# Performance work log

Hardware: AMD Instinct MI355X
Metric: run time of the kernel (lower is better)

Reference implementation:

```python
import jax, jax.numpy as jnp
import numpy as np

NUM_HEADS = 32
HEAD_DIM = 128
ROPE_THETA = 10000.0


def setup_inputs() -> dict:
    key = jax.random.key(0)
    k1, k2, k3 = jax.random.split(key, 3)
    B, S, H = 2, 2048, 4096
    scale = 0.02
    return {
        "x": jax.random.normal(k1, (B, S, H), dtype=jnp.float32),
        "Wqkv": jax.random.normal(k2, (H, 3 * H), dtype=jnp.float32) * scale,
        "Wo": jax.random.normal(k3, (H, H), dtype=jnp.float32) * scale,
    }


def _rope_cos_sin(seq_len, head_dim, dtype):
    # inv_freq over even dims, llama convention
    inv_freq = 1.0 / (ROPE_THETA ** (jnp.arange(0, head_dim, 2, dtype=jnp.float32) / head_dim))
    t = jnp.arange(seq_len, dtype=jnp.float32)
    freqs = jnp.outer(t, inv_freq)            # [S, hd/2]
    emb = jnp.concatenate([freqs, freqs], -1)  # [S, hd]
    return jnp.cos(emb).astype(dtype), jnp.sin(emb).astype(dtype)


def _rotate_half(v):
    v1, v2 = jnp.split(v, 2, axis=-1)
    return jnp.concatenate([-v2, v1], axis=-1)


def _apply_rope(q, k, cos, sin):
    # q,k: [B,S,nh,hd]; cos,sin: [S,hd] -> broadcast over B and heads
    cos = cos[None, :, None, :]
    sin = sin[None, :, None, :]
    q = q * cos + _rotate_half(q) * sin
    k = k * cos + _rotate_half(k) * sin
    return q, k


def reference(x, Wqkv, Wo):
    B, S, H = x.shape
    nh, hd = NUM_HEADS, HEAD_DIM
    scaling = 1.0 / jnp.sqrt(jnp.asarray(hd, dtype=x.dtype))

    qkv = jnp.einsum("bsh,hk->bsk", x, Wqkv)           # fused QKV proj
    q, k, v = jnp.split(qkv, 3, axis=-1)
    q = q.reshape(B, S, nh, hd)
    k = k.reshape(B, S, nh, hd)
    v = v.reshape(B, S, nh, hd)

    cos, sin = _rope_cos_sin(S, hd, x.dtype)
    q, k = _apply_rope(q, k, cos, sin)

    # causal scaled dot-product attention
    scores = jnp.einsum("bqnd,bknd->bnqk", q, k) * scaling  # [B,nh,S,S]
    causal = jnp.tril(jnp.ones((S, S), dtype=bool))
    scores = jnp.where(causal[None, None], scores, jnp.finfo(scores.dtype).min)
    probs = jax.nn.softmax(scores, axis=-1)
    ctx = jnp.einsum("bnqk,bknd->bqnd", probs, v).reshape(B, S, nh * hd)

    return jnp.einsum("bsh,ho->bso", ctx, Wo)
```

## Files before the change

kernel.cpp:

```cpp
#include <hip/hip_runtime.h>

typedef __bf16 v8bf __attribute__((ext_vector_type(8)));
typedef float  v4f  __attribute__((ext_vector_type(4)));

__device__ __forceinline__ float bf2f(unsigned short h) {
    union { unsigned int u; float f; } x; x.u = ((unsigned int)h) << 16; return x.f;
}
__device__ __forceinline__ unsigned short f2bf(float f) {
    union { float f; unsigned int u; } x; x.f = f;
    unsigned int u = x.u;
    u += 0x7fffu + ((u >> 16) & 1u);
    return (unsigned short)(u >> 16);
}
__device__ __forceinline__ void gll16(const void* g, void* l) {
    __builtin_amdgcn_global_load_lds((__attribute__((address_space(1))) void*)g,
                                     (__attribute__((address_space(3))) void*)l,
                                     16, 0, 0);
}

__global__ __launch_bounds__(256) void cvt_f32_bf16(
    const float* __restrict__ in, unsigned short* __restrict__ out)
{
    size_t i = ((size_t)blockIdx.x * 256 + threadIdx.x) * 4;
    float4 v = *(const float4*)&in[i];
    ushort4 o;
    o.x = f2bf(v.x); o.y = f2bf(v.y); o.z = f2bf(v.z); o.w = f2bf(v.w);
    *(ushort4*)&out[i] = o;
}

__global__ __launch_bounds__(256) void transpose_f32_bf16(
    const float* __restrict__ in, unsigned short* __restrict__ out, int ldIn, int M)
{
    __shared__ unsigned short t[64][68];
    const int c0 = blockIdx.x * 64, r0 = blockIdx.y * 64;
    const int lr = threadIdx.x >> 4;
    const int lc = (threadIdx.x & 15) * 4;
#pragma unroll
    for (int i = 0; i < 4; ++i) {
        int row = lr + i * 16;
        float4 v = *(const float4*)&in[(size_t)(r0 + row) * ldIn + c0 + lc];
        ushort4 o;
        o.x = f2bf(v.x); o.y = f2bf(v.y); o.z = f2bf(v.z); o.w = f2bf(v.w);
        *(ushort4*)&t[row][lc] = o;
    }
    __syncthreads();
#pragma unroll
    for (int i = 0; i < 4; ++i) {
        int orow = lr + i * 16;
        ushort4 v;
        v.x = t[lc + 0][orow]; v.y = t[lc + 1][orow];
        v.z = t[lc + 2][orow]; v.w = t[lc + 3][orow];
        *(ushort4*)&out[(size_t)(c0 + orow) * M + r0 + lc] = v;
    }
}

template <int MODE>
__global__ __launch_bounds__(512, 2) void gemm256(
    const unsigned short* __restrict__ A, const unsigned short* __restrict__ Bt,
    float* __restrict__ Cf, unsigned short* __restrict__ Ov, float postScale)
{
    constexpr int NT = 128;
    __shared__ unsigned short lA[4][8192];
    __shared__ unsigned short lB[4][8192];
    const int tid = threadIdx.x;
    const int wave = tid >> 6, lane = tid & 63;
    const int quad = lane >> 4, l16 = lane & 15;
    const int wr = wave >> 2, wc = wave & 3;

    const int bid = blockIdx.x;
    const int swz = (bid & 7) * 32 + (bid >> 3);
    const int m0 = (swz >> 4) * 256, n0 = (swz & 15) * 256;

    v4f acc[8][4] = {};

    const int sr0 = tid >> 2, sc0 = tid & 3;
    const int sr1 = 128 + sr0;
    const unsigned short* pA0 = A  + (size_t)(m0 + sr0) * 4096 + ((sc0 ^ ((sr0 >> 1) & 3)) << 3);
    const unsigned short* pA1 = A  + (size_t)(m0 + sr1) * 4096 + ((sc0 ^ ((sr1 >> 1) & 3)) << 3);
    const unsigned short* pB0 = Bt + (size_t)(n0 + sr0) * 4096 + ((sc0 ^ ((sr0 >> 1) & 3)) << 3);
    const unsigned short* pB1 = Bt + (size_t)(n0 + sr1) * 4096 + ((sc0 ^ ((sr1 >> 1) & 3)) << 3);

    {
        gll16(pA0, &lA[0][tid * 8]);  gll16(pA1, &lA[0][4096 + tid * 8]);
        gll16(pB0, &lB[0][tid * 8]);  gll16(pB1, &lB[0][4096 + tid * 8]);
        gll16(pA0 + 32, &lA[1][tid * 8]);  gll16(pA1 + 32, &lA[1][4096 + tid * 8]);
        gll16(pB0 + 32, &lB[1][tid * 8]);  gll16(pB1 + 32, &lB[1][4096 + tid * 8]);
        gll16(pA0 + 64, &lA[2][tid * 8]);  gll16(pA1 + 64, &lA[2][4096 + tid * 8]);
        gll16(pB0 + 64, &lB[2][tid * 8]);  gll16(pB1 + 64, &lB[2][4096 + tid * 8]);
    }
    asm volatile("s_waitcnt vmcnt(8)" ::: "memory");
    __builtin_amdgcn_s_barrier();

    const int swzk = (l16 >> 1) & 3;
    const int aoff = (wr * 128 + l16) * 32 + ((quad ^ swzk) << 3);
    const int boff = (wc * 16  + l16) * 32 + ((quad ^ swzk) << 3);

#pragma unroll 4
    for (int t = 0; t < NT; ++t) {
        const int cur = t & 3;
        const int nb = (t + 3) & 3;
        const size_t ko = (size_t)(t + 3) << 5;
        const bool pf = (t + 3 < NT);
        const unsigned short* lAc = &lA[cur][0];
        const unsigned short* lBc = &lB[cur][0];
        v8bf b[4], a0, a1;

        b[0] = *(const v8bf*)&lBc[boff];
        b[1] = *(const v8bf*)&lBc[boff + 2048];
        b[2] = *(const v8bf*)&lBc[boff + 4096];
        b[3] = *(const v8bf*)&lBc[boff + 6144];
        a0 = *(const v8bf*)&lAc[aoff];
        a1 = *(const v8bf*)&lAc[aoff + 512];
        if (pf) gll16(pA0 + ko, &lA[nb][tid * 8]);
        __builtin_amdgcn_s_barrier();
        __builtin_amdgcn_s_setprio(1);
#pragma unroll
        for (int ni = 0; ni < 4; ++ni) {
            acc[0][ni] = __builtin_amdgcn_mfma_f32_16x16x32_bf16(a0, b[ni], acc[0][ni], 0, 0, 0);
            acc[1][ni] = __builtin_amdgcn_mfma_f32_16x16x32_bf16(a1, b[ni], acc[1][ni], 0, 0, 0);
        }
        __builtin_amdgcn_s_setprio(0);

        a0 = *(const v8bf*)&lAc[aoff + 1024];
        a1 = *(const v8bf*)&lAc[aoff + 1536];
        if (pf) gll16(pA1 + ko, &lA[nb][4096 + tid * 8]);
        __builtin_amdgcn_s_barrier();
        __builtin_amdgcn_s_setprio(1);
#pragma unroll
        for (int ni = 0; ni < 4; ++ni) {
            acc[2][ni] = __builtin_amdgcn_mfma_f32_16x16x32_bf16(a0, b[ni], acc[2][ni], 0, 0, 0);
            acc[3][ni] = __builtin_amdgcn_mfma_f32_16x16x32_bf16(a1, b[ni], acc[3][ni], 0, 0, 0);
        }
        __builtin_amdgcn_s_setprio(0);

        a0 = *(const v8bf*)&lAc[aoff + 2048];
        a1 = *(const v8bf*)&lAc[aoff + 2560];
        if (pf) gll16(pB0 + ko, &lB[nb][tid * 8]);
        __builtin_amdgcn_s_barrier();
        __builtin_amdgcn_s_setprio(1);
#pragma unroll
        for (int ni = 0; ni < 4; ++ni) {
            acc[4][ni] = __builtin_amdgcn_mfma_f32_16x16x32_bf16(a0, b[ni], acc[4][ni], 0, 0, 0);
            acc[5][ni] = __builtin_amdgcn_mfma_f32_16x16x32_bf16(a1, b[ni], acc[5][ni], 0, 0, 0);
        }
        __builtin_amdgcn_s_setprio(0);

        a0 = *(const v8bf*)&lAc[aoff + 3072];
        a1 = *(const v8bf*)&lAc[aoff + 3584];
        if (pf) gll16(pB1 + ko, &lB[nb][4096 + tid * 8]);
        if (t < NT - 3)       asm volatile("s_waitcnt vmcnt(8)" ::: "memory");
        else if (t == NT - 3) asm volatile("s_waitcnt vmcnt(4)" ::: "memory");
        else if (t == NT - 2) asm volatile("s_waitcnt vmcnt(0)" ::: "memory");
        __builtin_amdgcn_s_barrier();
        __builtin_amdgcn_s_setprio(1);
#pragma unroll
        for (int ni = 0; ni < 4; ++ni) {
            acc[6][ni] = __builtin_amdgcn_mfma_f32_16x16x32_bf16(a0, b[ni], acc[6][ni], 0, 0, 0);
            acc[7][ni] = __builtin_amdgcn_mfma_f32_16x16x32_bf16(a1, b[ni], acc[7][ni], 0, 0, 0);
        }
        __builtin_amdgcn_s_setprio(0);
    }

    if (MODE == 0) {
#pragma unroll
        for (int mi = 0; mi < 8; ++mi) {
            int gm = m0 + wr * 128 + mi * 16 + quad * 4;
#pragma unroll
            for (int ni = 0; ni < 4; ++ni) {
                int gn = n0 + ni * 64 + wc * 16 + l16;
#pragma unroll
                for (int r = 0; r < 4; ++r)
                    Cf[(size_t)(gm + r) * 4096 + gn] = acc[mi][ni][r];
            }
        }
    } else if (MODE == 1) {
        const int d1 = wc * 16 + l16;
        const float inv = powf(10000.0f, -(float)d1 * 0.015625f);
        const int head0 = n0 >> 7;
#pragma unroll
        for (int mi = 0; mi < 8; ++mi) {
            int gmb = m0 + wr * 128 + mi * 16 + quad * 4;
            int b = gmb >> 11, sb = gmb & 2047;
            float sn[4], cs[4];
#pragma unroll
            for (int r = 0; r < 4; ++r)
                sincosf((float)(sb + r) * inv, &sn[r], &cs[r]);
#pragma unroll
            for (int hd = 0; hd < 2; ++hd) {
                size_t hb = ((size_t)(b * 32 + head0 + hd)) << 11;
#pragma unroll
                for (int r = 0; r < 4; ++r) {
                    float x1 = acc[mi][2 * hd][r], x2 = acc[mi][2 * hd + 1][r];
                    size_t adr = (hb + sb + r) << 7;
                    Ov[adr + d1]      = f2bf((x1 * cs[r] - x2 * sn[r]) * postScale);
                    Ov[adr + d1 + 64] = f2bf((x2 * cs[r] + x1 * sn[r]) * postScale);
                }
            }
        }
    } else {
        const int head0 = n0 >> 7;
#pragma unroll
        for (int mi = 0; mi < 8; ++mi) {
            int gmb = m0 + wr * 128 + mi * 16 + quad * 4;
            int b = gmb >> 11, s0 = gmb & 2047;
#pragma unroll
            for (int ni = 0; ni < 4; ++ni) {
                int head = head0 + (ni >> 1);
                int d = ((ni & 1) << 6) + wc * 16 + l16;
                ushort4 o;
                o.x = f2bf(acc[mi][ni][0]); o.y = f2bf(acc[mi][ni][1]);
                o.z = f2bf(acc[mi][ni][2]); o.w = f2bf(acc[mi][ni][3]);
                *(ushort4*)&Ov[(((size_t)(b * 32 + head)) << 18) +
                               ((size_t)d << 11) + s0] = o;
            }
        }
    }
}

__global__ __launch_bounds__(256, 5) void attn_kernel(
    const unsigned short* __restrict__ Q, const unsigned short* __restrict__ Kg,
    const unsigned short* __restrict__ Vt, unsigned short* __restrict__ ctx)
{
    __shared__ unsigned short lK[2][32 * 128];
    __shared__ unsigned short lV[2][128 * 32];

    const int qt  = gridDim.x - 1 - blockIdx.x;
    const int bh  = blockIdx.y;
    const int tid = threadIdx.x;
    const int wave = tid >> 6, lane = tid & 63;
    const int quad = lane >> 4, l16 = lane & 15;
    const int q0 = qt * 64;
    const size_t base = (size_t)bh << 18;

    auto stage = [&](int kv0, int buf) {
#pragma unroll
        for (int it = 0; it < 2; ++it) {
            int cid = it * 256 + tid;
            int row = cid >> 4, chk = cid & 15;
            gll16(Kg + base + ((size_t)(kv0 + row) << 7) + ((chk ^ (row & 15)) << 3),
                  &lK[buf][cid << 3]);
        }
#pragma unroll
        for (int it = 0; it < 2; ++it) {
            int cid = it * 256 + tid;
            int row = cid >> 2, chk = cid & 3;
            gll16(Vt + base + ((size_t)row << 11) + kv0 + ((chk ^ ((row >> 1) & 3)) << 3),
                  &lV[buf][cid << 3]);
        }
    };

    v8bf qf[4];
    {
        const unsigned short* qrow =
            Q + base + ((size_t)(q0 + wave * 16 + l16) << 7) + quad * 8;
#pragma unroll
        for (int kc = 0; kc < 4; ++kc)
            qf[kc] = *(const v8bf*)(qrow + kc * 32);
    }

    const int qg = q0 + wave * 16 + l16;
    float mrow = -1e30f, lrow = 0.f;
    v4f Oa[8] = {};
    const float c2 = 1.4426950408889634f;
    const float thr = 4.1589045f;

    const int nkt = 2 * qt + 2;
    stage(0, 0);
    for (int kt = 0; kt < nkt; ++kt) {
        const int cur = kt & 1;
        __syncthreads();
        if (kt + 1 < nkt) stage((kt + 1) * 32, cur ^ 1);

        const unsigned short* K_ = &lK[cur][0];
        const unsigned short* V_ = &lV[cur][0];
        const int kv0 = kt * 32;

        v4f sc[2] = {};
        __builtin_amdgcn_s_setprio(1);
#pragma unroll
        for (int kc = 0; kc < 4; ++kc) {
#pragma unroll
            for (int nt = 0; nt < 2; ++nt) {
                v8bf kf = *(const v8bf*)&K_[((nt * 16 + l16) << 7) +
                                            ((((kc << 2) + quad) ^ l16) << 3)];
                sc[nt] = __builtin_amdgcn_mfma_f32_16x16x32_bf16(kf, qf[kc], sc[nt], 0, 0, 0);
            }
        }
        __builtin_amdgcn_s_setprio(0);

        if (kt >= nkt - 2) {
#pragma unroll
            for (int nt = 0; nt < 2; ++nt) {
                int kvb = kv0 + nt * 16 + quad * 4;
#pragma unroll
                for (int r = 0; r < 4; ++r)
                    if (kvb + r > qg) sc[nt][r] = -1e30f;
            }
        }

        float tmax = fmaxf(fmaxf(fmaxf(sc[0][0], sc[0][1]), fmaxf(sc[0][2], sc[0][3])),
                           fmaxf(fmaxf(sc[1][0], sc[1][1]), fmaxf(sc[1][2], sc[1][3])));
        tmax = fmaxf(tmax, __shfl_xor(tmax, 16));
        tmax = fmaxf(tmax, __shfl_xor(tmax, 32));

        if (__ballot(tmax > mrow + thr) != 0ull) {
            float mnew = fmaxf(mrow, tmax);
            float alpha = exp2f((mrow - mnew) * c2);
            mrow = mnew;
            lrow *= alpha;
#pragma unroll
            for (int d8 = 0; d8 < 8; ++d8)
#pragma unroll
                for (int r = 0; r < 4; ++r)
                    Oa[d8][r] *= alpha;
        }
        const float mc = mrow * c2;
        float rsum = 0.f;
#pragma unroll
        for (int nt = 0; nt < 2; ++nt)
#pragma unroll
            for (int r = 0; r < 4; ++r) {
                float p = exp2f(fmaf(sc[nt][r], c2, -mc));
                sc[nt][r] = p;
                rsum += p;
            }
        rsum += __shfl_xor(rsum, 16);
        rsum += __shfl_xor(rsum, 32);
        lrow += rsum;

        unsigned int pk0[2], pk1[2];
#pragma unroll
        for (int h = 0; h < 2; ++h) {
            pk0[h] = (unsigned int)f2bf(sc[0][2 * h]) |
                     ((unsigned int)f2bf(sc[0][2 * h + 1]) << 16);
            pk1[h] = (unsigned int)f2bf(sc[1][2 * h]) |
                     ((unsigned int)f2bf(sc[1][2 * h + 1]) << 16);
        }
        union { unsigned int u[4]; v8bf v; } pu;
        const int sbase = ((quad & 1) << 5) + l16;
#pragma unroll
        for (int j2 = 0; j2 < 4; ++j2) {
            int src = sbase + ((j2 >> 1) << 4);
            int a = __shfl((int)pk0[j2 & 1], src);
            int b = __shfl((int)pk1[j2 & 1], src);
            pu.u[j2] = (quad < 2) ? (unsigned int)a : (unsigned int)b;
        }
        v8bf pf = pu.v;

        __builtin_amdgcn_s_setprio(1);
#pragma unroll
        for (int dt = 0; dt < 8; ++dt) {
            v8bf vf = *(const v8bf*)&V_[((dt * 16 + l16) << 5) +
                                        ((quad ^ ((l16 >> 1) & 3)) << 3)];
            Oa[dt] = __builtin_amdgcn_mfma_f32_16x16x32_bf16(vf, pf, Oa[dt], 0, 0, 0);
        }
        __builtin_amdgcn_s_setprio(0);
    }

    const int b = bh >> 5, h = bh & 31;
    const float invl = 1.0f / lrow;
    size_t rowb = ((size_t)(b * 2048 + qg) << 12) + ((size_t)h << 7);
#pragma unroll
    for (int dt = 0; dt < 8; ++dt) {
        ushort4 o;
        o.x = f2bf(Oa[dt][0] * invl);
        o.y = f2bf(Oa[dt][1] * invl);
        o.z = f2bf(Oa[dt][2] * invl);
        o.w = f2bf(Oa[dt][3] * invl);
        *(ushort4*)&ctx[rowb + dt * 16 + quad * 4] = o;
    }
}

extern "C" void kernel_launch(void* const* d_in, const int* in_sizes, int n_in,
                              void* d_out, int out_size, void* d_ws, size_t ws_size,
                              hipStream_t stream)
{
    const float* x    = (const float*)d_in[0];
    const float* Wqkv = (const float*)d_in[1];
    const float* Wo   = (const float*)d_in[2];
    float* out = (float*)d_out;

    char* ws = (char*)d_ws;
    const size_t B32 = (size_t)32 * 1024 * 1024;
    unsigned short* B0 = (unsigned short*)(ws);
    unsigned short* B1 = (unsigned short*)(ws + 1 * B32);
    unsigned short* B2 = (unsigned short*)(ws + 2 * B32);
    unsigned short* B3 = (unsigned short*)(ws + 3 * B32);
    unsigned short* B4 = (unsigned short*)(ws + 4 * B32);

    const float qscale = 0.08838834764831845f;

    cvt_f32_bf16<<<16384, 256, 0, stream>>>(x, B0);
    transpose_f32_bf16<<<dim3(64, 64), 256, 0, stream>>>(Wqkv, B4, 12288, 4096);
    gemm256<1><<<256, 512, 0, stream>>>(B0, B4, nullptr, B1, qscale);
    transpose_f32_bf16<<<dim3(64, 64), 256, 0, stream>>>(Wqkv + 4096, B4, 12288, 4096);
    gemm256<1><<<256, 512, 0, stream>>>(B0, B4, nullptr, B2, 1.0f);
    transpose_f32_bf16<<<dim3(64, 64), 256, 0, stream>>>(Wqkv + 8192, B4, 12288, 4096);
    gemm256<2><<<256, 512, 0, stream>>>(B0, B4, nullptr, B3, 1.0f);
    transpose_f32_bf16<<<dim3(64, 64), 256, 0, stream>>>(Wo, B4, 4096, 4096);
    attn_kernel<<<dim3(32, 64), 256, 0, stream>>>(B1, B2, B3, B0);
    gemm256<0><<<256, 512, 0, stream>>>(B0, B4, out, nullptr, 1.0f);
}
```

Before: 1.079 ms.

## Restructure GEMM main loop with 64-wide K tiles and half-tile double buffering

The bf16 GEMM mainloop now uses 64-element K steps (half the iterations), with LDS split into two buffers of A/B halves and an 8-way XOR swizzle. Each iteration runs four MFMA quadrants that reuse loaded A and B fragments, issuing global-to-LDS loads for the next tiles between phases. The goal is fewer barriers per unit of K and more MFMA work between loads. The cost is more registers per iteration and a shallower prefetch depth.

After: 1.066 ms. No clear change (-1.2%).

```diff
diff --git a/kernel.cpp b/kernel.cpp
--- a/kernel.cpp
+++ b/kernel.cpp
@@ -59,9 +59,9 @@
     const unsigned short* __restrict__ A, const unsigned short* __restrict__ Bt,
     float* __restrict__ Cf, unsigned short* __restrict__ Ov, float postScale)
 {
-    constexpr int NT = 128;
-    __shared__ unsigned short lA[4][8192];
-    __shared__ unsigned short lB[4][8192];
+    constexpr int NT = 64;
+    __shared__ unsigned short lA[4 * 8192];
+    __shared__ unsigned short lB[4 * 8192];
     const int tid = threadIdx.x;
     const int wave = tid >> 6, lane = tid & 63;
     const int quad = lane >> 4, l16 = lane & 15;
@@ -73,92 +73,127 @@
 
     v4f acc[8][4] = {};
 
-    const int sr0 = tid >> 2, sc0 = tid & 3;
-    const int sr1 = 128 + sr0;
-    const unsigned short* pA0 = A  + (size_t)(m0 + sr0) * 4096 + ((sc0 ^ ((sr0 >> 1) & 3)) << 3);
-    const unsigned short* pA1 = A  + (size_t)(m0 + sr1) * 4096 + ((sc0 ^ ((sr1 >> 1) & 3)) << 3);
-    const unsigned short* pB0 = Bt + (size_t)(n0 + sr0) * 4096 + ((sc0 ^ ((sr0 >> 1) & 3)) << 3);
-    const unsigned short* pB1 = Bt + (size_t)(n0 + sr1) * 4096 + ((sc0 ^ ((sr1 >> 1) & 3)) << 3);
-
-    {
-        gll16(pA0, &lA[0][tid * 8]);  gll16(pA1, &lA[0][4096 + tid * 8]);
-        gll16(pB0, &lB[0][tid * 8]);  gll16(pB1, &lB[0][4096 + tid * 8]);
-        gll16(pA0 + 32, &lA[1][tid * 8]);  gll16(pA1 + 32, &lA[1][4096 + tid * 8]);
-        gll16(pB0 + 32, &lB[1][tid * 8]);  gll16(pB1 + 32, &lB[1][4096 + tid * 8]);
-        gll16(pA0 + 64, &lA[2][tid * 8]);  gll16(pA1 + 64, &lA[2][4096 + tid * 8]);
-        gll16(pB0 + 64, &lB[2][tid * 8]);  gll16(pB1 + 64, &lB[2][4096 + tid * 8]);
-    }
-    asm volatile("s_waitcnt vmcnt(8)" ::: "memory");
+    const int srow = tid >> 3;
+    const int sof  = ((tid & 7) ^ (srow & 7)) << 3;
+    const unsigned short* pA[2][2]; const unsigned short* pB[2][2];
+#pragma unroll
+    for (int H = 0; H < 2; ++H)
+#pragma unroll
+        for (int i = 0; i < 2; ++i) {
+            pA[H][i] = A  + (size_t)(m0 + H * 128 + i * 64 + srow) * 4096 + sof;
+            pB[H][i] = Bt + (size_t)(n0 + H * 128 + i * 64 + srow) * 4096 + sof;
+        }
+    const int dst0 = tid * 8;
+
+    auto stA = [&](int H, int kt) {
+        unsigned short* d = &lA[((kt & 1) * 2 + H) * 8192 + dst0];
+        gll16(pA[H][0] + kt * 64, d);
+        gll16(pA[H][1] + kt * 64, d + 4096);
+    };
+    auto stB = [&](int H, int kt) {
+        unsigned short* d = &lB[((kt & 1) * 2 + H) * 8192 + dst0];
+        gll16(pB[H][0] + kt * 64, d);
+        gll16(pB[H][1] + kt * 64, d + 4096);
+    };
+
+    stB(0, 0); stB(1, 0); stA(0, 0); stA(1, 0);
+    stB(0, 1); stB(1, 1); stA(0, 1);
+    asm volatile("s_waitcnt vmcnt(6)" ::: "memory");
     __builtin_amdgcn_s_barrier();
 
-    const int swzk = (l16 >> 1) & 3;
-    const int aoff = (wr * 128 + l16) * 32 + ((quad ^ swzk) << 3);
-    const int boff = (wc * 16  + l16) * 32 + ((quad ^ swzk) << 3);
-
-#pragma unroll 4
+    const int cko0 = (quad ^ (l16 & 7)) << 3;
+    const int cko1 = ((4 + quad) ^ (l16 & 7)) << 3;
+    const int arow0 = l16 * 64;
+    const int brow0 = (wc * 16 + l16) * 64;
+
+#pragma unroll 2
     for (int t = 0; t < NT; ++t) {
-        const int cur = t & 3;
-        const int nb = (t + 3) & 3;
-        const size_t ko = (size_t)(t + 3) << 5;
-        const bool pf = (t + 3 < NT);
-        const unsigned short* lAc = &lA[cur][0];
-        const unsigned short* lBc = &lB[cur][0];
-        v8bf b[4], a0, a1;
-
-        b[0] = *(const v8bf*)&lBc[boff];
-        b[1] = *(const v8bf*)&lBc[boff + 2048];
-        b[2] = *(const v8bf*)&lBc[boff + 4096];
-        b[3] = *(const v8bf*)&lBc[boff + 6144];
-        a0 = *(const v8bf*)&lAc[aoff];
-        a1 = *(const v8bf*)&lAc[aoff + 512];
-        if (pf) gll16(pA0 + ko, &lA[nb][tid * 8]);
-        __builtin_amdgcn_s_barrier();
-        __builtin_amdgcn_s_setprio(1);
-#pragma unroll
-        for (int ni = 0; ni < 4; ++ni) {
-            acc[0][ni] = __builtin_amdgcn_mfma_f32_16x16x32_bf16(a0, b[ni], acc[0][ni], 0, 0, 0);
-            acc[1][ni] = __builtin_amdgcn_mfma_f32_16x16x32_bf16(a1, b[ni], acc[1][ni], 0, 0, 0);
-        }
-        __builtin_amdgcn_s_setprio(0);
-
-        a0 = *(const v8bf*)&lAc[aoff + 1024];
-        a1 = *(const v8bf*)&lAc[aoff + 1536];
-        if (pf) gll16(pA1 + ko, &lA[nb][4096 + tid * 8]);
-        __builtin_amdgcn_s_barrier();
-        __builtin_amdgcn_s_setprio(1);
-#pragma unroll
-        for (int ni = 0; ni < 4; ++ni) {
-            acc[2][ni] = __builtin_amdgcn_mfma_f32_16x16x32_bf16(a0, b[ni], acc[2][ni], 0, 0, 0);
-            acc[3][ni] = __builtin_amdgcn_mfma_f32_16x16x32_bf16(a1, b[ni], acc[3][ni], 0, 0, 0);
-        }
-        __builtin_amdgcn_s_setprio(0);
-
-        a0 = *(const v8bf*)&lAc[aoff + 2048];
-        a1 = *(const v8bf*)&lAc[aoff + 2560];
-        if (pf) gll16(pB0 + ko, &lB[nb][tid * 8]);
-        __builtin_amdgcn_s_barrier();
-        __builtin_amdgcn_s_setprio(1);
-#pragma unroll
-        for (int ni = 0; ni < 4; ++ni) {
-            acc[4][ni] = __builtin_amdgcn_mfma_f32_16x16x32_bf16(a0, b[ni], acc[4][ni], 0, 0, 0);
-            acc[5][ni] = __builtin_amdgcn_mfma_f32_16x16x32_bf16(a1, b[ni], acc[5][ni], 0, 0, 0);
-        }
-        __builtin_amdgcn_s_setprio(0);
-
-        a0 = *(const v8bf*)&lAc[aoff + 3072];
-        a1 = *(const v8bf*)&lAc[aoff + 3584];
-        if (pf) gll16(pB1 + ko, &lB[nb][4096 + tid * 8]);
-        if (t < NT - 3)       asm volatile("s_waitcnt vmcnt(8)" ::: "memory");
-        else if (t == NT - 3) asm volatile("s_waitcnt vmcnt(4)" ::: "memory");
-        else if (t == NT - 2) asm volatile("s_waitcnt vmcnt(0)" ::: "memory");
-        __builtin_amdgcn_s_barrier();
-        __builtin_amdgcn_s_setprio(1);
-#pragma unroll
-        for (int ni = 0; ni < 4; ++ni) {
-            acc[6][ni] = __builtin_amdgcn_mfma_f32_16x16x32_bf16(a0, b[ni], acc[6][ni], 0, 0, 0);
-            acc[7][ni] = __builtin_amdgcn_mfma_f32_16x16x32_bf16(a1, b[ni], acc[7][ni], 0, 0, 0);
-        }
-        __builtin_amdgcn_s_setprio(0);
+        const int c = t & 1;
+        const unsigned short* lAc = &lA[(c * 2 + wr) * 8192];
+        const unsigned short* lB0 = &lB[(c * 2 + 0) * 8192];
+        const unsigned short* lB1 = &lB[(c * 2 + 1) * 8192];
+        v8bf a[4][2], b0[2][2], b1[2][2];
+
+#pragma unroll
+        for (int mi = 0; mi < 4; ++mi) {
+            a[mi][0] = *(const v8bf*)&lAc[arow0 + mi * 1024 + cko0];
+            a[mi][1] = *(const v8bf*)&lAc[arow0 + mi * 1024 + cko1];
+        }
+#pragma unroll
+        for (int ni = 0; ni < 2; ++ni) {
+            b0[ni][0] = *(const v8bf*)&lB0[brow0 + ni * 4096 + cko0];
+            b0[ni][1] = *(const v8bf*)&lB0[brow0 + ni * 4096 + cko1];
+        }
+        if (t + 1 < NT) stA(1, t + 1);
+        __builtin_amdgcn_s_barrier();
+        __builtin_amdgcn_s_setprio(1);
+#pragma unroll
+        for (int kc = 0; kc < 2; ++kc)
+#pragma unroll
+            for (int mi = 0; mi < 4; ++mi)
+#pragma unroll
+                for (int ni = 0; ni < 2; ++ni)
+                    acc[mi][ni] = __builtin_amdgcn_mfma_f32_16x16x32_bf16(
+                        a[mi][kc], b0[ni][kc], acc[mi][ni], 0, 0, 0);
+        __builtin_amdgcn_s_setprio(0);
+        __builtin_amdgcn_s_barrier();
+
+#pragma unroll
+        for (int ni = 0; ni < 2; ++ni) {
+            b1[ni][0] = *(const v8bf*)&lB1[brow0 + ni * 4096 + cko0];
+            b1[ni][1] = *(const v8bf*)&lB1[brow0 + ni * 4096 + cko1];
+        }
+        if (t + 2 < NT) stB(0, t + 2);
+        __builtin_amdgcn_s_barrier();
+        __builtin_amdgcn_s_setprio(1);
+#pragma unroll
+        for (int kc = 0; kc < 2; ++kc)
+#pragma unroll
+            for (int mi = 0; mi < 4; ++mi)
+#pragma unroll
+                for (int ni = 0; ni < 2; ++ni)
+                    acc[mi][2 + ni] = __builtin_amdgcn_mfma_f32_16x16x32_bf16(
+                        a[mi][kc], b1[ni][kc], acc[mi][2 + ni], 0, 0, 0);
+        __builtin_amdgcn_s_setprio(0);
+        __builtin_amdgcn_s_barrier();
+
+#pragma unroll
+        for (int mi = 0; mi < 4; ++mi) {
+            a[mi][0] = *(const v8bf*)&lAc[arow0 + (4 + mi) * 1024 + cko0];
+            a[mi][1] = *(const v8bf*)&lAc[arow0 + (4 + mi) * 1024 + cko1];
+        }
+        if (t + 2 < NT) stB(1, t + 2);
+        __builtin_amdgcn_s_barrier();
+        __builtin_amdgcn_s_setprio(1);
+#pragma unroll
+        for (int kc = 0; kc < 2; ++kc)
+#pragma unroll
+            for (int mi = 0; mi < 4; ++mi)
+#pragma unroll
+                for (int ni = 0; ni < 2; ++ni)
+                    acc[4 + mi][2 + ni] = __builtin_amdgcn_mfma_f32_16x16x32_bf16(
+                        a[mi][kc], b1[ni][kc], acc[4 + mi][2 + ni], 0, 0, 0);
+        __builtin_amdgcn_s_setprio(0);
+        __builtin_amdgcn_s_barrier();
+
+        if (t + 2 < NT) {
+            stA(0, t + 2);
+            asm volatile("s_waitcnt vmcnt(6)" ::: "memory");
+        } else if (t + 1 < NT) {
+            asm volatile("s_waitcnt vmcnt(0)" ::: "memory");
+        }
+        __builtin_amdgcn_s_barrier();
+        __builtin_amdgcn_s_setprio(1);
+#pragma unroll
+        for (int kc = 0; kc < 2; ++kc)
+#pragma unroll
+            for (int mi = 0; mi < 4; ++mi)
+#pragma unroll
+                for (int ni = 0; ni < 2; ++ni)
+                    acc[4 + mi][ni] = __builtin_amdgcn_mfma_f32_16x16x32_bf16(
+                        a[mi][kc], b0[ni][kc], acc[4 + mi][ni], 0, 0, 0);
+        __builtin_amdgcn_s_setprio(0);
+        __builtin_amdgcn_s_barrier();
     }
 
     if (MODE == 0) {
```
